# Kernel optimization log

Measured on AMD Instinct MI355X. Metric: run time of the kernel, lower is better.

Reference implementation:

```python
import jax, jax.numpy as jnp
import numpy as np

B, S, D = 4, 2048, 1024
H, DK = 16, 64           # n_heads, d_kv; inner_dim = H*DK = 1024 = D
R = 16
SCALING = 32.0 / R       # lora_alpha / r = 2.0


def setup_inputs() -> dict:
    key = jax.random.key(0)
    ks = jax.random.split(key, 10)
    inner = H * DK
    sd = 1.0 / np.sqrt(D)
    return {
        "hidden_states": jax.random.normal(ks[0], (B, S, D), jnp.float32),
        "position_bias": jax.random.normal(ks[1], (1, H, S, S), jnp.float32),
        "Wq": jax.random.normal(ks[2], (inner, D), jnp.float32) * sd,
        "Wk": jax.random.normal(ks[3], (inner, D), jnp.float32) * sd,
        "Wv": jax.random.normal(ks[4], (inner, D), jnp.float32) * sd,
        "Wo": jax.random.normal(ks[5], (D, inner), jnp.float32) * sd,
        "Aq": jax.random.normal(ks[6], (R, D), jnp.float32) * sd,
        "Bq": jax.random.normal(ks[7], (inner, R), jnp.float32) * 0.01,
        "Av": jax.random.normal(ks[8], (R, D), jnp.float32) * sd,
        "Bv": jax.random.normal(ks[9], (inner, R), jnp.float32) * 0.01,
    }


def reference(hidden_states, position_bias, Wq, Wk, Wv, Wo, Aq, Bq, Av, Bv):
    x = hidden_states  # [B,S,D]

    def lora(w_a, w_b):
        # ((x @ A^T) @ B^T) * scaling; low-rank path, rank R
        return ((x @ w_a.T) @ w_b.T) * SCALING

    def heads(t):  # [B,S,H*DK] -> [B,H,S,DK]
        return t.reshape(B, S, H, DK).transpose(0, 2, 1, 3)

    q = heads(x @ Wq.T + lora(Aq, Bq))
    k = heads(x @ Wk.T)
    v = heads(x @ Wv.T + lora(Av, Bv))

    # T5-style: no 1/sqrt(d) scaling; additive position bias
    scores = jnp.einsum("bhqd,bhkd->bhqk", q, k) + position_bias
    attn = jax.nn.softmax(scores, axis=-1)
    out = jnp.einsum("bhqk,bhkd->bhqd", attn, v)
    out = out.transpose(0, 2, 1, 3).reshape(B, S, H * DK)
    return out @ Wo.T
```

## Files before the change

kernel.cpp:

```cpp
#include <hip/hip_runtime.h>
#include <hip/hip_bf16.h>

typedef __bf16 bf16x8 __attribute__((ext_vector_type(8)));
typedef float  f32x4  __attribute__((ext_vector_type(4)));
typedef float  f32x16 __attribute__((ext_vector_type(16)));
typedef unsigned u32x2 __attribute__((ext_vector_type(2)));
typedef unsigned u32x4 __attribute__((ext_vector_type(4)));
typedef unsigned short u16;
typedef unsigned u32;
typedef unsigned long long u64;

#define L2E 1.44269504089f

__device__ __forceinline__ u16 f2b(float f) {
    __bf16 h = (__bf16)f;
    return __builtin_bit_cast(u16, h);
}

typedef const __attribute__((address_space(1))) void* gas1_t;
typedef __attribute__((address_space(3))) void* las3_t;

__device__ __forceinline__ void gl_lds16(const void* g, void* l) {
    __builtin_amdgcn_global_load_lds((gas1_t)g, (las3_t)l, 16, 0, 0);
}


__global__ void cvt_bf16(const float* __restrict__ in, u16* __restrict__ out, int n4) {
    int i = blockIdx.x * 256 + threadIdx.x;
    if (i < n4) {
        float4 v = ((const float4*)in)[i];
        u64 pk = (u64)f2b(v.x) | ((u64)f2b(v.y) << 16) | ((u64)f2b(v.z) << 32) | ((u64)f2b(v.w) << 48);
        ((u64*)out)[i] = pk;
    }
}

__global__ void prep_wqkv(const float* __restrict__ Wq, const float* __restrict__ Wk,
                          const float* __restrict__ Wv, const float* __restrict__ Aq,
                          const float* __restrict__ Bq, const float* __restrict__ Av,
                          const float* __restrict__ Bv, u16* __restrict__ out) {
    int idx = blockIdx.x * 256 + threadIdx.x;
    int n = idx >> 10, j = idx & 1023;
    float v;
    if (n < 1024) {
        v = Wq[n * 1024 + j];
        const float* Br = Bq + n * 16;
        float s = 0.f;
#pragma unroll
        for (int r = 0; r < 16; ++r) s += Br[r] * Aq[r * 1024 + j];
        v += 2.0f * s;
    } else if (n < 2048) {
        v = Wk[(n - 1024) * 1024 + j];
    } else {
        int nn = n - 2048;
        v = Wv[nn * 1024 + j];
        const float* Br = Bv + nn * 16;
        float s = 0.f;
#pragma unroll
        for (int r = 0; r < 16; ++r) s += Br[r] * Av[r * 1024 + j];
        v += 2.0f * s;
    }
    out[idx] = f2b(v);
}


template <int EPI>
__global__ __launch_bounds__(256, 2)
void gemm_bt(const u16* __restrict__ A, const u16* __restrict__ W,
             float* __restrict__ Cout,
             u16* __restrict__ qo, u16* __restrict__ ko, u16* __restrict__ vo,
             int M, int N, int K) {
    __shared__ u16 ldsA[128 * 32];
    __shared__ u16 ldsW[128 * 32];
    const int t = threadIdx.x;
    const int l = t & 63;
    const int m0 = blockIdx.y * 128;
    const int n0 = blockIdx.x * 128;
    const int wm = (t >> 6) >> 1, wn = (t >> 6) & 1;
    const int lc = l & 15, lg = l >> 4;

    const int srow = t >> 2;
    const int sby = ((t & 3) * 16) ^ ((srow & 3) << 4);
    const size_t Ar0 = (size_t)(m0 + srow) * K, Ar1 = (size_t)(m0 + srow + 64) * K;
    const size_t Wr0 = (size_t)(n0 + srow) * K, Wr1 = (size_t)(n0 + srow + 64) * K;
    char* dA = (char*)ldsA;
    char* dW = (char*)ldsW;
    const int d0 = srow * 64 + (t & 3) * 16;
    const int d1 = d0 + 4096;

    f32x4 acc[4][4];
#pragma unroll
    for (int i = 0; i < 4; ++i)
#pragma unroll
        for (int j = 0; j < 4; ++j) acc[i][j] = (f32x4)0.f;

    for (int kt = 0; kt < K; kt += 32) {
        const size_t kb = (size_t)kt * 2;
        gl_lds16((const char*)A + Ar0 * 2 + kb + sby, dA + d0);
        gl_lds16((const char*)A + Ar1 * 2 + kb + sby, dA + d1);
        gl_lds16((const char*)W + Wr0 * 2 + kb + sby, dW + d0);
        gl_lds16((const char*)W + Wr1 * 2 + kb + sby, dW + d1);
        __syncthreads();
        bf16x8 af[4], wf[4];
#pragma unroll
        for (int mi = 0; mi < 4; ++mi) {
            int row = wm * 64 + mi * 16 + lc;
            af[mi] = *(const bf16x8*)(dA + row * 64 + ((lg * 16) ^ ((row & 3) << 4)));
        }
#pragma unroll
        for (int ni = 0; ni < 4; ++ni) {
            int row = wn * 64 + ni * 16 + lc;
            wf[ni] = *(const bf16x8*)(dW + row * 64 + ((lg * 16) ^ ((row & 3) << 4)));
        }
#pragma unroll
        for (int mi = 0; mi < 4; ++mi)
#pragma unroll
            for (int ni = 0; ni < 4; ++ni)
                acc[mi][ni] = __builtin_amdgcn_mfma_f32_16x16x32_bf16(af[mi], wf[ni], acc[mi][ni], 0, 0, 0);
        __syncthreads();
    }

    if (EPI == 0) {
#pragma unroll
        for (int mi = 0; mi < 4; ++mi) {
            int row = m0 + wm * 64 + mi * 16 + lg * 4;
#pragma unroll
            for (int ni = 0; ni < 4; ++ni) {
                int col = n0 + wn * 64 + ni * 16 + lc;
#pragma unroll
                for (int r = 0; r < 4; ++r)
                    Cout[(size_t)(row + r) * N + col] = acc[mi][ni][r];
            }
        }
    } else {
#pragma unroll
        for (int mi = 0; mi < 4; ++mi) {
#pragma unroll
            for (int ni = 0; ni < 4; ++ni) {
                int n = n0 + wn * 64 + ni * 16 + lc;
                int which = n >> 10, inner = n & 1023;
                int h = inner >> 6, dk = inner & 63;
#pragma unroll
                for (int r = 0; r < 4; ++r) {
                    int mrow = m0 + wm * 64 + mi * 16 + lg * 4 + r;
                    int b = mrow >> 11, s = mrow & 2047;
                    size_t bh = (size_t)(b * 16 + h);
                    float av = acc[mi][ni][r];
                    if (which == 0)      qo[(bh * 2048 + s) * 64 + dk] = f2b(av * L2E);
                    else if (which == 1) ko[(bh * 2048 + s) * 64 + dk] = f2b(av);
                    else                 vo[(bh * 64 + dk) * 2048 + s] = f2b(av);
                }
            }
        }
    }
}


__global__ __launch_bounds__(256, 3)
void attn(const u16* __restrict__ Qg, const u16* __restrict__ Kg,
          const u16* __restrict__ Vg, const float* __restrict__ bias,
          u16* __restrict__ Og) {
    __shared__ u16 Kb[2][4096];
    __shared__ u16 Vb[2][4096];
    const int t = threadIdx.x;
    const int l = t & 63;
    const int w = t >> 6;
    const int bid = ((blockIdx.x & 7) << 7) | (blockIdx.x >> 3);
    const int h = bid & 15, b = (bid >> 4) & 3, qt = bid >> 6;
    const int q0 = qt * 128 + w * 32;
    const int l31 = l & 31, L5 = l >> 5;
    const int rkey = (l & 7) << 4;
    const size_t bh = (size_t)b * 16 + h;
    const u16* Qp = Qg + bh * 2048 * 64;
    const char* Kpb = (const char*)(Kg + bh * 2048 * 64);
    const char* Vpb = (const char*)(Vg + bh * 64 * 2048);

    const int row0 = w * 8 + (l >> 3);
    const int row1 = row0 + 32;
    const int scol2 = ((l & 7) * 16) ^ (((l >> 3) & 7) << 4);
    const int ldst = w * 1024 + l * 16;

    gl_lds16(Kpb + (size_t)row0 * 128 + scol2, (char*)Kb[0] + ldst);
    gl_lds16(Kpb + (size_t)row1 * 128 + scol2, (char*)Kb[0] + 4096 + ldst);
    gl_lds16(Vpb + (size_t)row0 * 4096 + scol2, (char*)Vb[0] + ldst);
    gl_lds16(Vpb + (size_t)row1 * 4096 + scol2, (char*)Vb[0] + 4096 + ldst);
    asm volatile("" ::: "memory");

    bf16x8 qf[4];
#pragma unroll
    for (int d = 0; d < 4; ++d)
        qf[d] = *(const bf16x8*)&Qp[(size_t)(q0 + l31) * 64 + d * 16 + L5 * 8];

    f32x16 acc[2];
#pragma unroll
    for (int o = 0; o < 2; ++o) acc[o] = (f32x16)0.f;
    f32x4 lsum4 = (f32x4)0.f;

    const float* bp0 = bias + ((size_t)h * 2048 + q0 + l31) * 2048 + 4 * L5;
    float4 br[2][4];
#pragma unroll
    for (int ni = 0; ni < 2; ++ni)
#pragma unroll
        for (int blk = 0; blk < 4; ++blk)
            br[ni][blk] = *(const float4*)(bp0 + ni * 32 + blk * 8);

    asm volatile("s_waitcnt vmcnt(8)\n\ts_barrier" ::: "memory");

    for (int kt = 0; kt < 32; ++kt) {
        const int cur = kt & 1;
        const int k0 = kt * 64;

        if (kt < 31) {
            const size_t kb = (size_t)(k0 + 64);
            gl_lds16(Kpb + (kb + row0) * 128 + scol2, (char*)Kb[cur ^ 1] + ldst);
            gl_lds16(Kpb + (kb + row1) * 128 + scol2, (char*)Kb[cur ^ 1] + 4096 + ldst);
            gl_lds16(Vpb + (size_t)row0 * 4096 + kb * 2 + scol2, (char*)Vb[cur ^ 1] + ldst);
            gl_lds16(Vpb + (size_t)row1 * 4096 + kb * 2 + scol2, (char*)Vb[cur ^ 1] + 4096 + ldst);
        }
        asm volatile("" ::: "memory");

        f32x16 sfr[2];
#pragma unroll
        for (int ni = 0; ni < 2; ++ni) {
            bf16x8 kf[4];
#pragma unroll
            for (int d = 0; d < 4; ++d)
                kf[d] = *(const bf16x8*)((const char*)Kb[cur] + (ni * 32 + l31) * 128 + ((d * 32 + L5 * 16) ^ rkey));
            __builtin_amdgcn_s_setprio(1);
            sfr[ni] = __builtin_amdgcn_mfma_f32_32x32x16_bf16(kf[0], qf[0], (f32x16)0.f, 0, 0, 0);
#pragma unroll
            for (int d = 1; d < 4; ++d)
                sfr[ni] = __builtin_amdgcn_mfma_f32_32x32x16_bf16(kf[d], qf[d], sfr[ni], 0, 0, 0);
            __builtin_amdgcn_s_setprio(0);
        }

        u32 Dv[2][4][2];
#pragma unroll
        for (int ni = 0; ni < 2; ++ni)
#pragma unroll
            for (int blk = 0; blk < 4; ++blk) {
                f32x4 pv;
#pragma unroll
                for (int off = 0; off < 4; ++off)
                    pv[off] = __builtin_amdgcn_exp2f(fmaf((&br[ni][blk].x)[off], L2E, sfr[ni][blk * 4 + off]));
                lsum4 += pv;
                asm("v_cvt_pk_bf16_f32 %0, %1, %2" : "=v"(Dv[ni][blk][0]) : "v"(pv[0]), "v"(pv[1]));
                asm("v_cvt_pk_bf16_f32 %0, %1, %2" : "=v"(Dv[ni][blk][1]) : "v"(pv[2]), "v"(pv[3]));
            }

        u32x4 pw[4];
#pragma unroll
        for (int ni = 0; ni < 2; ++ni)
#pragma unroll
            for (int ke = 0; ke < 2; ++ke)
#pragma unroll
                for (int c = 0; c < 2; ++c) {
                    u32x2 r = __builtin_amdgcn_permlane32_swap(Dv[ni][2 * ke][c], Dv[ni][2 * ke + 1][c], false, false);
                    pw[ni * 2 + ke][c] = r[0];
                    pw[ni * 2 + ke][2 + c] = r[1];
                }
        bf16x8 pf[4];
#pragma unroll
        for (int ks = 0; ks < 4; ++ks) pf[ks] = __builtin_bit_cast(bf16x8, pw[ks]);

        if (kt < 31) {
#pragma unroll
            for (int ni = 0; ni < 2; ++ni)
#pragma unroll
                for (int blk = 0; blk < 4; ++blk)
                    br[ni][blk] = *(const float4*)(bp0 + k0 + 64 + ni * 32 + blk * 8);
        }

#pragma unroll
        for (int o = 0; o < 2; ++o) {
            bf16x8 vf[4];
#pragma unroll
            for (int ks = 0; ks < 4; ++ks)
                vf[ks] = *(const bf16x8*)((const char*)Vb[cur] + (o * 32 + l31) * 128 + ((ks * 32 + L5 * 16) ^ rkey));
            __builtin_amdgcn_s_setprio(1);
#pragma unroll
            for (int ks = 0; ks < 4; ++ks)
                acc[o] = __builtin_amdgcn_mfma_f32_32x32x16_bf16(pf[ks], vf[ks], acc[o], 0, 0, 0);
            __builtin_amdgcn_s_setprio(0);
        }

        asm volatile("s_waitcnt vmcnt(8)\n\ts_barrier" ::: "memory");
    }

    float ls = (lsum4[0] + lsum4[1]) + (lsum4[2] + lsum4[3]);
    ls += __shfl_xor(ls, 32);
    float inv = 1.0f / ls;
    float invr[16];
#pragma unroll
    for (int r = 0; r < 16; ++r)
        invr[r] = __shfl(inv, (r & 3) + 8 * (r >> 2) + 4 * L5);

#pragma unroll
    for (int o = 0; o < 2; ++o)
#pragma unroll
        for (int r = 0; r < 16; ++r) {
            int rowr = (r & 3) + 8 * (r >> 2) + 4 * L5;
            Og[((size_t)b * 2048 + q0 + rowr) * 1024 + h * 64 + o * 32 + l31] = f2b(acc[o][r] * invr[r]);
        }
}


extern "C" void kernel_launch(void* const* d_in, const int* in_sizes, int n_in,
                              void* d_out, int out_size, void* d_ws, size_t ws_size,
                              hipStream_t stream) {
    const float* x    = (const float*)d_in[0];
    const float* bias = (const float*)d_in[1];
    const float* Wq   = (const float*)d_in[2];
    const float* Wk   = (const float*)d_in[3];
    const float* Wv   = (const float*)d_in[4];
    const float* Wo   = (const float*)d_in[5];
    const float* Aq   = (const float*)d_in[6];
    const float* Bq   = (const float*)d_in[7];
    const float* Av   = (const float*)d_in[8];
    const float* Bv   = (const float*)d_in[9];
    float* out = (float*)d_out;

    char* ws = (char*)d_ws;
    u16* xb   = (u16*)(ws);
    u16* wqkv = (u16*)(ws + (16ull << 20));
    u16* wob  = (u16*)(ws + (22ull << 20));
    u16* qw   = (u16*)(ws + (24ull << 20));
    u16* kw   = (u16*)(ws + (40ull << 20));
    u16* vw   = (u16*)(ws + (56ull << 20));

    cvt_bf16<<<8192, 256, 0, stream>>>(x, xb, 2097152);
    cvt_bf16<<<1024, 256, 0, stream>>>(Wo, wob, 262144);
    prep_wqkv<<<12288, 256, 0, stream>>>(Wq, Wk, Wv, Aq, Bq, Av, Bv, wqkv);
    gemm_bt<1><<<dim3(24, 64), 256, 0, stream>>>(xb, wqkv, nullptr, qw, kw, vw, 8192, 3072, 1024);
    attn<<<1024, 256, 0, stream>>>(qw, kw, vw, bias, xb);
    gemm_bt<0><<<dim3(8, 64), 256, 0, stream>>>(xb, wob, out, nullptr, nullptr, nullptr, 8192, 1024, 1024);
}
```

Baseline: 327.8 us.

## Triple-buffer K/V tiles in LDS and issue bias prefetch earlier

Grows the K and V shared-memory buffers from two to three stages, so tiles are prefetched two iterations ahead. The buffer indices rotate in a loop that is no longer unrolled, and the wait count is relaxed to match. The bias add is folded into the score registers right after the QK MFMAs, which lets the next tile's bias loads be issued before the softmax and permute work rather than after. This aims to hide more global-load latency, at the cost of 50% more LDS per block, which could reduce occupancy or add pressure.

```diff
diff --git a/kernel.cpp b/kernel.cpp
--- a/kernel.cpp
+++ b/kernel.cpp
@@ -159,8 +159,8 @@
 void attn(const u16* __restrict__ Qg, const u16* __restrict__ Kg,
           const u16* __restrict__ Vg, const float* __restrict__ bias,
           u16* __restrict__ Og) {
-    __shared__ u16 Kb[2][4096];
-    __shared__ u16 Vb[2][4096];
+    __shared__ u16 Kb[3][4096];
+    __shared__ u16 Vb[3][4096];
     const int t = threadIdx.x;
     const int l = t & 63;
     const int w = t >> 6;
@@ -183,12 +183,17 @@
     gl_lds16(Kpb + (size_t)row1 * 128 + scol2, (char*)Kb[0] + 4096 + ldst);
     gl_lds16(Vpb + (size_t)row0 * 4096 + scol2, (char*)Vb[0] + ldst);
     gl_lds16(Vpb + (size_t)row1 * 4096 + scol2, (char*)Vb[0] + 4096 + ldst);
+    gl_lds16(Kpb + (size_t)(64 + row0) * 128 + scol2, (char*)Kb[1] + ldst);
+    gl_lds16(Kpb + (size_t)(64 + row1) * 128 + scol2, (char*)Kb[1] + 4096 + ldst);
+    gl_lds16(Vpb + (size_t)row0 * 4096 + 128 + scol2, (char*)Vb[1] + ldst);
+    gl_lds16(Vpb + (size_t)row1 * 4096 + 128 + scol2, (char*)Vb[1] + 4096 + ldst);
     asm volatile("" ::: "memory");
 
     bf16x8 qf[4];
 #pragma unroll
     for (int d = 0; d < 4; ++d)
         qf[d] = *(const bf16x8*)&Qp[(size_t)(q0 + l31) * 64 + d * 16 + L5 * 8];
+    asm volatile("" ::: "memory");
 
     f32x16 acc[2];
 #pragma unroll
@@ -205,16 +210,18 @@
 
     asm volatile("s_waitcnt vmcnt(8)\n\ts_barrier" ::: "memory");
 
+    int i0 = 0, i1 = 1, i2 = 2;
+
+#pragma unroll 1
     for (int kt = 0; kt < 32; ++kt) {
-        const int cur = kt & 1;
         const int k0 = kt * 64;
 
-        if (kt < 31) {
-            const size_t kb = (size_t)(k0 + 64);
-            gl_lds16(Kpb + (kb + row0) * 128 + scol2, (char*)Kb[cur ^ 1] + ldst);
-            gl_lds16(Kpb + (kb + row1) * 128 + scol2, (char*)Kb[cur ^ 1] + 4096 + ldst);
-            gl_lds16(Vpb + (size_t)row0 * 4096 + kb * 2 + scol2, (char*)Vb[cur ^ 1] + ldst);
-            gl_lds16(Vpb + (size_t)row1 * 4096 + kb * 2 + scol2, (char*)Vb[cur ^ 1] + 4096 + ldst);
+        if (kt < 30) {
+            const size_t kb = (size_t)(k0 + 128);
+            gl_lds16(Kpb + (kb + row0) * 128 + scol2, (char*)Kb[i2] + ldst);
+            gl_lds16(Kpb + (kb + row1) * 128 + scol2, (char*)Kb[i2] + 4096 + ldst);
+            gl_lds16(Vpb + (size_t)row0 * 4096 + kb * 2 + scol2, (char*)Vb[i2] + ldst);
+            gl_lds16(Vpb + (size_t)row1 * 4096 + kb * 2 + scol2, (char*)Vb[i2] + 4096 + ldst);
         }
         asm volatile("" ::: "memory");
 
@@ -224,7 +231,7 @@
             bf16x8 kf[4];
 #pragma unroll
             for (int d = 0; d < 4; ++d)
-                kf[d] = *(const bf16x8*)((const char*)Kb[cur] + (ni * 32 + l31) * 128 + ((d * 32 + L5 * 16) ^ rkey));
+                kf[d] = *(const bf16x8*)((const char*)Kb[i0] + (ni * 32 + l31) * 128 + ((d * 32 + L5 * 16) ^ rkey));
             __builtin_amdgcn_s_setprio(1);
             sfr[ni] = __builtin_amdgcn_mfma_f32_32x32x16_bf16(kf[0], qf[0], (f32x16)0.f, 0, 0, 0);
 #pragma unroll
@@ -233,6 +240,22 @@
             __builtin_amdgcn_s_setprio(0);
         }
 
+#pragma unroll
+        for (int ni = 0; ni < 2; ++ni)
+#pragma unroll
+            for (int blk = 0; blk < 4; ++blk)
+#pragma unroll
+                for (int off = 0; off < 4; ++off)
+                    sfr[ni][blk * 4 + off] = fmaf((&br[ni][blk].x)[off], L2E, sfr[ni][blk * 4 + off]);
+
+        if (kt < 31) {
+#pragma unroll
+            for (int ni = 0; ni < 2; ++ni)
+#pragma unroll
+                for (int blk = 0; blk < 4; ++blk)
+                    br[ni][blk] = *(const float4*)(bp0 + k0 + 64 + ni * 32 + blk * 8);
+        }
+
         u32 Dv[2][4][2];
 #pragma unroll
         for (int ni = 0; ni < 2; ++ni)
@@ -241,7 +264,7 @@
                 f32x4 pv;
 #pragma unroll
                 for (int off = 0; off < 4; ++off)
-                    pv[off] = __builtin_amdgcn_exp2f(fmaf((&br[ni][blk].x)[off], L2E, sfr[ni][blk * 4 + off]));
+                    pv[off] = __builtin_amdgcn_exp2f(sfr[ni][blk * 4 + off]);
                 lsum4 += pv;
                 asm("v_cvt_pk_bf16_f32 %0, %1, %2" : "=v"(Dv[ni][blk][0]) : "v"(pv[0]), "v"(pv[1]));
                 asm("v_cvt_pk_bf16_f32 %0, %1, %2" : "=v"(Dv[ni][blk][1]) : "v"(pv[2]), "v"(pv[3]));
@@ -262,20 +285,12 @@
 #pragma unroll
         for (int ks = 0; ks < 4; ++ks) pf[ks] = __builtin_bit_cast(bf16x8, pw[ks]);
 
-        if (kt < 31) {
-#pragma unroll
-            for (int ni = 0; ni < 2; ++ni)
-#pragma unroll
-                for (int blk = 0; blk < 4; ++blk)
-                    br[ni][blk] = *(const float4*)(bp0 + k0 + 64 + ni * 32 + blk * 8);
-        }
-
 #pragma unroll
         for (int o = 0; o < 2; ++o) {
             bf16x8 vf[4];
 #pragma unroll
             for (int ks = 0; ks < 4; ++ks)
-                vf[ks] = *(const bf16x8*)((const char*)Vb[cur] + (o * 32 + l31) * 128 + ((ks * 32 + L5 * 16) ^ rkey));
+                vf[ks] = *(const bf16x8*)((const char*)Vb[i0] + (o * 32 + l31) * 128 + ((ks * 32 + L5 * 16) ^ rkey));
             __builtin_amdgcn_s_setprio(1);
 #pragma unroll
             for (int ks = 0; ks < 4; ++ks)
@@ -283,7 +298,9 @@
             __builtin_amdgcn_s_setprio(0);
         }
 
-        asm volatile("s_waitcnt vmcnt(8)\n\ts_barrier" ::: "memory");
+        asm volatile("s_waitcnt vmcnt(12)\n\ts_barrier" ::: "memory");
+
+        int tmp = i0; i0 = i1; i1 = i2; i2 = tmp;
     }
 
     float ls = (lsum4[0] + lsum4[1]) + (lsum4[2] + lsum4[3]);
```

Result: no change. 332.0 us (+1.3%).

## Raise attention occupancy by streaming bias per half-tile and cutting register use

Applied to the files above, without the earlier changes.

Raises the attention kernel's launch bound from 3 to 4 blocks per SIMD and cuts register pressure to fit. The bias prefetch into registers one tile ahead is removed; each 32-key half-tile now loads its bias just before use. The score/softmax work is split into two sequential halves, the loop is kept rolled, and the inline-asm bf16 pack is replaced by per-value conversions. The aim is more waves in flight to hide latency. The cost is exposed bias-load latency, a barrier that now waits for all loads (vmcnt 0) and so drains the K/V prefetch every iteration, and possibly slower conversion code.

```diff
diff --git a/kernel.cpp b/kernel.cpp
--- a/kernel.cpp
+++ b/kernel.cpp
@@ -155,7 +155,7 @@
 }
 
 
-__global__ __launch_bounds__(256, 3)
+__global__ __launch_bounds__(256, 4)
 void attn(const u16* __restrict__ Qg, const u16* __restrict__ Kg,
           const u16* __restrict__ Vg, const float* __restrict__ bias,
           u16* __restrict__ Og) {
@@ -183,7 +183,6 @@
     gl_lds16(Kpb + (size_t)row1 * 128 + scol2, (char*)Kb[0] + 4096 + ldst);
     gl_lds16(Vpb + (size_t)row0 * 4096 + scol2, (char*)Vb[0] + ldst);
     gl_lds16(Vpb + (size_t)row1 * 4096 + scol2, (char*)Vb[0] + 4096 + ldst);
-    asm volatile("" ::: "memory");
 
     bf16x8 qf[4];
 #pragma unroll
@@ -196,18 +195,19 @@
     f32x4 lsum4 = (f32x4)0.f;
 
     const float* bp0 = bias + ((size_t)h * 2048 + q0 + l31) * 2048 + 4 * L5;
-    float4 br[2][4];
-#pragma unroll
-    for (int ni = 0; ni < 2; ++ni)
-#pragma unroll
-        for (int blk = 0; blk < 4; ++blk)
-            br[ni][blk] = *(const float4*)(bp0 + ni * 32 + blk * 8);
-
-    asm volatile("s_waitcnt vmcnt(8)\n\ts_barrier" ::: "memory");
-
+
+    asm volatile("s_waitcnt vmcnt(0)\n\ts_barrier" ::: "memory");
+
+#pragma unroll 1
     for (int kt = 0; kt < 32; ++kt) {
         const int cur = kt & 1;
         const int k0 = kt * 64;
+
+        float4 br0[4];
+#pragma unroll
+        for (int blk = 0; blk < 4; ++blk)
+            br0[blk] = *(const float4*)(bp0 + k0 + blk * 8);
+        asm volatile("" ::: "memory");
 
         if (kt < 31) {
             const size_t kb = (size_t)(k0 + 64);
@@ -218,56 +218,86 @@
         }
         asm volatile("" ::: "memory");
 
-        f32x16 sfr[2];
-#pragma unroll
-        for (int ni = 0; ni < 2; ++ni) {
+        bf16x8 pf[4];
+
+        {
+            f32x16 sfr;
             bf16x8 kf[4];
 #pragma unroll
             for (int d = 0; d < 4; ++d)
-                kf[d] = *(const bf16x8*)((const char*)Kb[cur] + (ni * 32 + l31) * 128 + ((d * 32 + L5 * 16) ^ rkey));
+                kf[d] = *(const bf16x8*)((const char*)Kb[cur] + (l31) * 128 + ((d * 32 + L5 * 16) ^ rkey));
             __builtin_amdgcn_s_setprio(1);
-            sfr[ni] = __builtin_amdgcn_mfma_f32_32x32x16_bf16(kf[0], qf[0], (f32x16)0.f, 0, 0, 0);
+            sfr = __builtin_amdgcn_mfma_f32_32x32x16_bf16(kf[0], qf[0], (f32x16)0.f, 0, 0, 0);
 #pragma unroll
             for (int d = 1; d < 4; ++d)
-                sfr[ni] = __builtin_amdgcn_mfma_f32_32x32x16_bf16(kf[d], qf[d], sfr[ni], 0, 0, 0);
+                sfr = __builtin_amdgcn_mfma_f32_32x32x16_bf16(kf[d], qf[d], sfr, 0, 0, 0);
             __builtin_amdgcn_s_setprio(0);
-        }
-
-        u32 Dv[2][4][2];
-#pragma unroll
-        for (int ni = 0; ni < 2; ++ni)
+
+            u32 Dv[4][2];
 #pragma unroll
             for (int blk = 0; blk < 4; ++blk) {
                 f32x4 pv;
 #pragma unroll
                 for (int off = 0; off < 4; ++off)
-                    pv[off] = __builtin_amdgcn_exp2f(fmaf((&br[ni][blk].x)[off], L2E, sfr[ni][blk * 4 + off]));
+                    pv[off] = __builtin_amdgcn_exp2f(fmaf((&br0[blk].x)[off], L2E, sfr[blk * 4 + off]));
                 lsum4 += pv;
-                asm("v_cvt_pk_bf16_f32 %0, %1, %2" : "=v"(Dv[ni][blk][0]) : "v"(pv[0]), "v"(pv[1]));
-                asm("v_cvt_pk_bf16_f32 %0, %1, %2" : "=v"(Dv[ni][blk][1]) : "v"(pv[2]), "v"(pv[3]));
-            }
-
-        u32x4 pw[4];
-#pragma unroll
-        for (int ni = 0; ni < 2; ++ni)
-#pragma unroll
-            for (int ke = 0; ke < 2; ++ke)
+                Dv[blk][0] = (u32)f2b(pv[0]) | ((u32)f2b(pv[1]) << 16);
+                Dv[blk][1] = (u32)f2b(pv[2]) | ((u32)f2b(pv[3]) << 16);
+            }
+#pragma unroll
+            for (int ke = 0; ke < 2; ++ke) {
+                u32x4 pwv;
 #pragma unroll
                 for (int c = 0; c < 2; ++c) {
-                    u32x2 r = __builtin_amdgcn_permlane32_swap(Dv[ni][2 * ke][c], Dv[ni][2 * ke + 1][c], false, false);
-                    pw[ni * 2 + ke][c] = r[0];
-                    pw[ni * 2 + ke][2 + c] = r[1];
+                    u32x2 rr = __builtin_amdgcn_permlane32_swap(Dv[2 * ke][c], Dv[2 * ke + 1][c], false, false);
+                    pwv[c] = rr[0];
+                    pwv[2 + c] = rr[1];
                 }
-        bf16x8 pf[4];
-#pragma unroll
-        for (int ks = 0; ks < 4; ++ks) pf[ks] = __builtin_bit_cast(bf16x8, pw[ks]);
-
-        if (kt < 31) {
-#pragma unroll
-            for (int ni = 0; ni < 2; ++ni)
-#pragma unroll
-                for (int blk = 0; blk < 4; ++blk)
-                    br[ni][blk] = *(const float4*)(bp0 + k0 + 64 + ni * 32 + blk * 8);
+                pf[ke] = __builtin_bit_cast(bf16x8, pwv);
+            }
+        }
+
+        float4 br1[4];
+#pragma unroll
+        for (int blk = 0; blk < 4; ++blk)
+            br1[blk] = *(const float4*)(bp0 + k0 + 32 + blk * 8);
+        asm volatile("" ::: "memory");
+
+        {
+            f32x16 sfr;
+            bf16x8 kf[4];
+#pragma unroll
+            for (int d = 0; d < 4; ++d)
+                kf[d] = *(const bf16x8*)((const char*)Kb[cur] + (32 + l31) * 128 + ((d * 32 + L5 * 16) ^ rkey));
+            __builtin_amdgcn_s_setprio(1);
+            sfr = __builtin_amdgcn_mfma_f32_32x32x16_bf16(kf[0], qf[0], (f32x16)0.f, 0, 0, 0);
+#pragma unroll
+            for (int d = 1; d < 4; ++d)
+                sfr = __builtin_amdgcn_mfma_f32_32x32x16_bf16(kf[d], qf[d], sfr, 0, 0, 0);
+            __builtin_amdgcn_s_setprio(0);
+
+            u32 Dv[4][2];
+#pragma unroll
+            for (int blk = 0; blk < 4; ++blk) {
+                f32x4 pv;
+#pragma unroll
+                for (int off = 0; off < 4; ++off)
+                    pv[off] = __builtin_amdgcn_exp2f(fmaf((&br1[blk].x)[off], L2E, sfr[blk * 4 + off]));
+                lsum4 += pv;
+                Dv[blk][0] = (u32)f2b(pv[0]) | ((u32)f2b(pv[1]) << 16);
+                Dv[blk][1] = (u32)f2b(pv[2]) | ((u32)f2b(pv[3]) << 16);
+            }
+#pragma unroll
+            for (int ke = 0; ke < 2; ++ke) {
+                u32x4 pwv;
+#pragma unroll
+                for (int c = 0; c < 2; ++c) {
+                    u32x2 rr = __builtin_amdgcn_permlane32_swap(Dv[2 * ke][c], Dv[2 * ke + 1][c], false, false);
+                    pwv[c] = rr[0];
+                    pwv[2 + c] = rr[1];
+                }
+                pf[2 + ke] = __builtin_bit_cast(bf16x8, pwv);
+            }
         }
 
 #pragma unroll
@@ -283,7 +313,7 @@
             __builtin_amdgcn_s_setprio(0);
         }
 
-        asm volatile("s_waitcnt vmcnt(8)\n\ts_barrier" ::: "memory");
+        asm volatile("s_waitcnt vmcnt(0)\n\ts_barrier" ::: "memory");
     }
 
     float ls = (lsum4[0] + lsum4[1]) + (lsum4[2] + lsum4[3]);
```

Measured after the change: 331.0 us. Within noise of the previous version (+1.0%).
